# Kernel optimization log

Hardware: AMD Instinct MI355X
Metric: run time of the kernel (lower is better)

Reference implementation:

```python
import jax, jax.numpy as jnp
import numpy as np

EPS = 1e-3  # finite-difference step from __init__ (eps=0.001)


def setup_inputs() -> dict:
    key = jax.random.key(0)
    k1, k2, k3 = jax.random.split(key, 3)
    B, L, C = 8, 1024, 8192  # L = 32*32 token grid, C = VQ codebook size
    logits = jax.random.normal(k1, (B, L, C), dtype=jnp.float32)
    mask = jax.random.randint(k2, (B, L), 0, 2).astype(bool)
    target_signature = jax.random.normal(k3, (B, 2), dtype=jnp.float32)
    return {"logits": logits, "mask": mask, "target_signature": target_signature}


def reference(logits, mask, target_signature):
    # gudhi.CubicalComplex(img).betti_numbers() computes the Betti numbers of the
    # FULL 2D cubical complex (independent of cell values): always [b0=1, b1=0].
    # So the per-sample signature is the constant [1, 0] and the softmax/argmax
    # chain in the original forward does not influence the output.
    B, L, C = logits.shape
    sig = jnp.broadcast_to(jnp.array([1.0, 0.0], dtype=logits.dtype), (B, 2))
    err2 = (sig - target_signature) ** 2
    loss = jnp.mean(err2)                    # F.mse_loss(signatures, target)
    per_b = jnp.mean(err2, axis=-1)          # F.mse_loss(sig_p, target[b]) per sample
    # Finite-difference: perturbing any masked logit leaves sig_p == [1,0], so
    # grad[b,l,c] = (per_b[b] - loss) / eps at masked positions, 0 elsewhere.
    diff = (per_b - loss) / EPS              # [B]
    grad = jnp.where(mask[:, :, None], diff[:, None, None],
                     jnp.zeros((), logits.dtype))
    grad = jnp.broadcast_to(grad, (B, L, C)).astype(logits.dtype)
    return loss, grad
```

## Files before the change

### kernel.cpp

```cpp
#include <hip/hip_runtime.h>


#define B_DIM 8
#define L_DIM 1024
#define C_DIM 8192
#define NROWS (B_DIM * L_DIM)
#define EPS_INV 1000.0f

__global__ void topo_prep(const void* __restrict__ mask_raw,
                          const float* __restrict__ target,
                          float* __restrict__ rowval)
{
    int r = blockIdx.x * blockDim.x + threadIdx.x;
    if (r >= NROWS) return;

    const unsigned int* mw = (const unsigned int*)mask_raw;
    bool byte_mode = false;
#pragma unroll
    for (int i = 0; i < 32; ++i) {
        if (mw[i] & 0xFFFFFF00u) byte_mode = true;
    }

    float loss = 0.0f;
#pragma unroll
    for (int b = 0; b < B_DIM; ++b) {
        float t0 = target[2 * b];
        float t1 = target[2 * b + 1];
        float e0 = 1.0f - t0;
        loss += e0 * e0 + t1 * t1;
    }
    loss *= (1.0f / 16.0f);

    int b = r >> 10;
    float t0 = target[2 * b];
    float t1 = target[2 * b + 1];
    float e0 = 1.0f - t0;
    float per_b = 0.5f * (e0 * e0 + t1 * t1);
    float diff = (per_b - loss) * EPS_INV;

    int mval = byte_mode ? (int)((const unsigned char*)mask_raw)[r]
                         : ((const int*)mask_raw)[r];
    rowval[r] = mval ? diff : 0.0f;
    if (r == 0) rowval[NROWS] = loss;
}

__global__ void topo_fill(const float* __restrict__ rowval,
                          float* __restrict__ out,
                          long long M)
{
    long long stride = (long long)gridDim.x * blockDim.x;
    for (long long m = (long long)blockIdx.x * blockDim.x + threadIdx.x;
         m < M; m += stride) {
        long long g = m << 2;
        float val = rowval[g >> 13];
        float vx;
        if (m == 0) {
            vx = rowval[NROWS];
        } else if ((g & (C_DIM - 1)) == 0) {
            vx = rowval[(g - 1) >> 13];
        } else {
            vx = val;
        }
        float4 v = make_float4(vx, val, val, val);
        *reinterpret_cast<float4*>(out + g) = v;
        if (m == M - 1) {
            out[M << 2] = rowval[NROWS - 1];
        }
    }
}

extern "C" void kernel_launch(void* const* d_in, const int* in_sizes, int n_in,
                              void* d_out, int out_size, void* d_ws, size_t ws_size,
                              hipStream_t stream) {
    const void*  mask   = d_in[1];
    const float* target = (const float*)d_in[2];
    float* rowval = (float*)d_ws;
    float* out    = (float*)d_out;

    topo_prep<<<NROWS / 256, 256, 0, stream>>>(mask, target, rowval);

    long long M = ((long long)out_size - 1) >> 2;
    topo_fill<<<4096, 256, 0, stream>>>(rowval, out, M);
}
```

Before: 46.61 us.

## Fuse prep and fill kernels into one launch with nontemporal stores

Merges the row-value prep kernel into the fill kernel. Each block computes the per-sample diffs and the loss into shared memory, and each thread reads the mask byte directly. This removes one kernel launch and the workspace round trip, and it switches the output writes to nontemporal stores and halves the grid size. In exchange every block recomputes the small target reduction and re-reads the mask words, and the lower block count may change how well the write bandwidth is saturated.

```diff
diff --git a/kernel.cpp b/kernel.cpp
--- a/kernel.cpp
+++ b/kernel.cpp
@@ -7,12 +7,37 @@
 #define NROWS (B_DIM * L_DIM)
 #define EPS_INV 1000.0f
 
-__global__ void topo_prep(const void* __restrict__ mask_raw,
-                          const float* __restrict__ target,
-                          float* __restrict__ rowval)
+typedef float f32x4 __attribute__((ext_vector_type(4)));
+
+__global__ void topo_fused(const void* __restrict__ mask_raw,
+                           const float* __restrict__ target,
+                           float* __restrict__ out,
+                           long long M)
 {
-    int r = blockIdx.x * blockDim.x + threadIdx.x;
-    if (r >= NROWS) return;
+    __shared__ float s_diff[9];
+
+    if (threadIdx.x == 0) {
+        float pb0, pb1, pb2, pb3, pb4, pb5, pb6, pb7;
+        float loss = 0.0f;
+        {
+            float t0, t1, e0;
+#define PB(i, dst) t0 = target[2*(i)]; t1 = target[2*(i)+1]; e0 = 1.0f - t0; \
+                   dst = 0.5f * (e0*e0 + t1*t1); loss += dst;
+            PB(0, pb0) PB(1, pb1) PB(2, pb2) PB(3, pb3)
+            PB(4, pb4) PB(5, pb5) PB(6, pb6) PB(7, pb7)
+#undef PB
+        }
+        loss *= (1.0f / 8.0f);
+        s_diff[0] = (pb0 - loss) * EPS_INV;
+        s_diff[1] = (pb1 - loss) * EPS_INV;
+        s_diff[2] = (pb2 - loss) * EPS_INV;
+        s_diff[3] = (pb3 - loss) * EPS_INV;
+        s_diff[4] = (pb4 - loss) * EPS_INV;
+        s_diff[5] = (pb5 - loss) * EPS_INV;
+        s_diff[6] = (pb6 - loss) * EPS_INV;
+        s_diff[7] = (pb7 - loss) * EPS_INV;
+        s_diff[8] = loss;
+    }
 
     const unsigned int* mw = (const unsigned int*)mask_raw;
     bool byte_mode = false;
@@ -20,51 +45,37 @@
     for (int i = 0; i < 32; ++i) {
         if (mw[i] & 0xFFFFFF00u) byte_mode = true;
     }
+    const unsigned char* mb = (const unsigned char*)mask_raw;
+    const int*           mi = (const int*)mask_raw;
 
-    float loss = 0.0f;
-#pragma unroll
-    for (int b = 0; b < B_DIM; ++b) {
-        float t0 = target[2 * b];
-        float t1 = target[2 * b + 1];
-        float e0 = 1.0f - t0;
-        loss += e0 * e0 + t1 * t1;
-    }
-    loss *= (1.0f / 16.0f);
+    __syncthreads();
 
-    int b = r >> 10;
-    float t0 = target[2 * b];
-    float t1 = target[2 * b + 1];
-    float e0 = 1.0f - t0;
-    float per_b = 0.5f * (e0 * e0 + t1 * t1);
-    float diff = (per_b - loss) * EPS_INV;
-
-    int mval = byte_mode ? (int)((const unsigned char*)mask_raw)[r]
-                         : ((const int*)mask_raw)[r];
-    rowval[r] = mval ? diff : 0.0f;
-    if (r == 0) rowval[NROWS] = loss;
-}
-
-__global__ void topo_fill(const float* __restrict__ rowval,
-                          float* __restrict__ out,
-                          long long M)
-{
     long long stride = (long long)gridDim.x * blockDim.x;
     for (long long m = (long long)blockIdx.x * blockDim.x + threadIdx.x;
          m < M; m += stride) {
         long long g = m << 2;
-        float val = rowval[g >> 13];
-        float vx;
-        if (m == 0) {
-            vx = rowval[NROWS];
-        } else if ((g & (C_DIM - 1)) == 0) {
-            vx = rowval[(g - 1) >> 13];
-        } else {
-            vx = val;
+        int row = (int)(g >> 13);
+        int mval = byte_mode ? (int)mb[row] : mi[row];
+        float val = mval ? s_diff[row >> 10] : 0.0f;
+
+        float vx = val;
+        if ((g & (C_DIM - 1)) == 0) {
+            if (m == 0) {
+                vx = s_diff[8];
+            } else {
+                int prow = row - 1;
+                int pmval = byte_mode ? (int)mb[prow] : mi[prow];
+                vx = pmval ? s_diff[prow >> 10] : 0.0f;
+            }
         }
-        float4 v = make_float4(vx, val, val, val);
-        *reinterpret_cast<float4*>(out + g) = v;
+
+        f32x4 v = {vx, val, val, val};
+        __builtin_nontemporal_store(v, reinterpret_cast<f32x4*>(out + g));
+
         if (m == M - 1) {
-            out[M << 2] = rowval[NROWS - 1];
+            int lrow = NROWS - 1;
+            int lmval = byte_mode ? (int)mb[lrow] : mi[lrow];
+            out[M << 2] = lmval ? s_diff[7] : 0.0f;
         }
     }
 }
@@ -74,11 +85,9 @@
                               hipStream_t stream) {
     const void*  mask   = d_in[1];
     const float* target = (const float*)d_in[2];
-    float* rowval = (float*)d_ws;
-    float* out    = (float*)d_out;
-
-    topo_prep<<<NROWS / 256, 256, 0, stream>>>(mask, target, rowval);
+    float* out = (float*)d_out;
 
     long long M = ((long long)out_size - 1) >> 2;
-    topo_fill<<<4096, 256, 0, stream>>>(rowval, out, M);
+
+    topo_fused<<<2048, 256, 0, stream>>>(mask, target, out, M);
 }
```

Result: slower. 51.55 us (+10.6%).

## Fuse mask prep into fill kernel with per-block row ownership

Applied to the files above, without the earlier changes.

Merges the row-value prep kernel into the fill kernel. Each block now owns two output rows and computes the loss and masked diff values itself, so the workspace round trip and the second launch are gone. Stores are unrolled with fixed per-thread offsets instead of a grid-stride loop with per-element index math. In exchange every block redundantly reads the target and mask words, and the layout is hard-coded to the fixed shape.

```diff
diff --git a/kernel.cpp b/kernel.cpp
--- a/kernel.cpp
+++ b/kernel.cpp
@@ -4,15 +4,36 @@
 #define B_DIM 8
 #define L_DIM 1024
 #define C_DIM 8192
-#define NROWS (B_DIM * L_DIM)
+#define NROWS 8192
 #define EPS_INV 1000.0f
+#define CHUNKS_PER_ROW 2048
+#define BLOCKS 4096
+#define TPB 256
 
-__global__ void topo_prep(const void* __restrict__ mask_raw,
-                          const float* __restrict__ target,
-                          float* __restrict__ rowval)
+__device__ __forceinline__ float per_b_val(const float* __restrict__ target, int i) {
+    float t0 = target[2 * i], t1 = target[2 * i + 1];
+    float e0 = 1.0f - t0;
+    return 0.5f * (e0 * e0 + t1 * t1);
+}
+
+__global__ void __launch_bounds__(TPB)
+topo_fill2(const void* __restrict__ mask_raw,
+           const float* __restrict__ target,
+           float* __restrict__ out)
 {
-    int r = blockIdx.x * blockDim.x + threadIdx.x;
-    if (r >= NROWS) return;
+    int b = blockIdx.x;
+    int t = threadIdx.x;
+    int r0 = 2 * b, r1 = r0 + 1;
+
+    float loss = 0.0f;
+#pragma unroll
+    for (int i = 0; i < 8; ++i) loss += per_b_val(target, i);
+    loss *= 0.125f;
+
+    int bidx = r0 >> 10;
+    float diff0 = (per_b_val(target, bidx) - loss) * EPS_INV;
+    int prow = (r0 > 0) ? r0 - 1 : 0;
+    float diffp = (per_b_val(target, prow >> 10) - loss) * EPS_INV;
 
     const unsigned int* mw = (const unsigned int*)mask_raw;
     bool byte_mode = false;
@@ -20,52 +41,36 @@
     for (int i = 0; i < 32; ++i) {
         if (mw[i] & 0xFFFFFF00u) byte_mode = true;
     }
+    const unsigned char* mb = (const unsigned char*)mask_raw;
+    const int*           mi = (const int*)mask_raw;
 
-    float loss = 0.0f;
+    int m0 = byte_mode ? (int)mb[r0]   : mi[r0];
+    int m1 = byte_mode ? (int)mb[r1]   : mi[r1];
+    int mp = byte_mode ? (int)mb[prow] : mi[prow];
+
+    float val0 = m0 ? diff0 : 0.0f;
+    float val1 = m1 ? diff0 : 0.0f;
+    float valp = mp ? diffp : 0.0f;
+
+    float* p = out + (((long long)b * (2 * CHUNKS_PER_ROW) + t) << 2);
+
 #pragma unroll
-    for (int b = 0; b < B_DIM; ++b) {
-        float t0 = target[2 * b];
-        float t1 = target[2 * b + 1];
-        float e0 = 1.0f - t0;
-        loss += e0 * e0 + t1 * t1;
+    for (int it = 0; it < 8; ++it) {
+        float vx = val0;
+        if (it == 0 && t == 0) vx = (b == 0) ? loss : valp;
+        float4 v = make_float4(vx, val0, val0, val0);
+        *reinterpret_cast<float4*>(p + (long long)it * (TPB * 4)) = v;
     }
-    loss *= (1.0f / 16.0f);
+#pragma unroll
+    for (int it = 8; it < 16; ++it) {
+        float vx = val1;
+        if (it == 8 && t == 0) vx = val0;
+        float4 v = make_float4(vx, val1, val1, val1);
+        *reinterpret_cast<float4*>(p + (long long)it * (TPB * 4)) = v;
+    }
 
-    int b = r >> 10;
-    float t0 = target[2 * b];
-    float t1 = target[2 * b + 1];
-    float e0 = 1.0f - t0;
-    float per_b = 0.5f * (e0 * e0 + t1 * t1);
-    float diff = (per_b - loss) * EPS_INV;
-
-    int mval = byte_mode ? (int)((const unsigned char*)mask_raw)[r]
-                         : ((const int*)mask_raw)[r];
-    rowval[r] = mval ? diff : 0.0f;
-    if (r == 0) rowval[NROWS] = loss;
-}
-
-__global__ void topo_fill(const float* __restrict__ rowval,
-                          float* __restrict__ out,
-                          long long M)
-{
-    long long stride = (long long)gridDim.x * blockDim.x;
-    for (long long m = (long long)blockIdx.x * blockDim.x + threadIdx.x;
-         m < M; m += stride) {
-        long long g = m << 2;
-        float val = rowval[g >> 13];
-        float vx;
-        if (m == 0) {
-            vx = rowval[NROWS];
-        } else if ((g & (C_DIM - 1)) == 0) {
-            vx = rowval[(g - 1) >> 13];
-        } else {
-            vx = val;
-        }
-        float4 v = make_float4(vx, val, val, val);
-        *reinterpret_cast<float4*>(out + g) = v;
-        if (m == M - 1) {
-            out[M << 2] = rowval[NROWS - 1];
-        }
+    if (b == BLOCKS - 1 && t == TPB - 1) {
+        out[(long long)NROWS * C_DIM] = val1;
     }
 }
 
@@ -74,11 +79,7 @@
                               hipStream_t stream) {
     const void*  mask   = d_in[1];
     const float* target = (const float*)d_in[2];
-    float* rowval = (float*)d_ws;
-    float* out    = (float*)d_out;
+    float* out = (float*)d_out;
 
-    topo_prep<<<NROWS / 256, 256, 0, stream>>>(mask, target, rowval);
-
-    long long M = ((long long)out_size - 1) >> 2;
-    topo_fill<<<4096, 256, 0, stream>>>(rowval, out, M);
+    topo_fill2<<<BLOCKS, TPB, 0, stream>>>(mask, target, out);
 }
```

Measured after the change: 41.39 us. 11.2% less time.
